# Kernel optimization log

Hardware: AMD Instinct MI355X
Metric: run time of the kernel (lower is better)

Reference implementation:

```python
import jax, jax.numpy as jnp
import numpy as np

EMBED = 768
DIM = 800          # embed + 32 gender features
IN_C = 1024
GRID = 32          # img_size // patch_size(=1)
LN_EPS = 1e-5      # torch nn.LayerNorm default


def setup_inputs() -> dict:
    key = jax.random.key(0)
    ks = jax.random.split(key, 8)
    B = 32
    x = jax.random.normal(ks[0], (B, IN_C, GRID, GRID), dtype=jnp.float32)
    gender_encode = jax.random.normal(ks[1], (B, 32), dtype=jnp.float32)
    # PatchEmbed 1x1 conv (acts as per-pixel linear) + LayerNorm params
    conv_w = jax.random.normal(ks[2], (EMBED, IN_C), dtype=jnp.float32) * (IN_C ** -0.5)
    conv_b = jnp.zeros((EMBED,), dtype=jnp.float32)
    ln_g = jnp.ones((EMBED,), dtype=jnp.float32)
    ln_b = jnp.zeros((EMBED,), dtype=jnp.float32)
    cls_token = jax.random.normal(ks[3], (1, 1, EMBED), dtype=jnp.float32) * 0.02
    # Attention qkv linear (bias=True); proj is never used in the forward path
    qkv_w = jax.random.normal(ks[4], (3 * DIM, DIM), dtype=jnp.float32) * (DIM ** -0.5)
    qkv_b = jnp.zeros((3 * DIM,), dtype=jnp.float32)
    return {
        "x": x, "gender_encode": gender_encode,
        "conv_w": conv_w, "conv_b": conv_b,
        "ln_g": ln_g, "ln_b": ln_b,
        "cls_token": cls_token,
        "qkv_w": qkv_w, "qkv_b": qkv_b,
    }


def _forward(x, gender_encode, conv_w, conv_b, ln_g, ln_b, cls_token, qkv_w, qkv_b):
    B = x.shape[0]
    # PatchEmbed: 1x1 conv stride 1 == per-pixel linear; flatten(2).transpose(1,2)
    p = jnp.einsum('bchw,oc->bhwo', x, conv_w) + conv_b        # [B,32,32,768]
    p = p.reshape(B, GRID * GRID, EMBED)                        # [B,1024,768]
    mu = jnp.mean(p, axis=-1, keepdims=True)
    var = jnp.mean((p - mu) ** 2, axis=-1, keepdims=True)
    p = (p - mu) * jax.lax.rsqrt(var + LN_EPS) * ln_g + ln_b
    # prepend cls token, concat broadcast gender features
    cls = jnp.broadcast_to(cls_token, (B, 1, EMBED))
    t = jnp.concatenate([cls, p], axis=1)                       # [B,1025,768]
    g = jnp.broadcast_to(gender_encode[:, None, :], (B, t.shape[1], 32))
    t = jnp.concatenate([t, g], axis=2)                         # [B,1025,800]
    # Attention (note: self.norm / proj / v are unused in the original forward)
    qkv = t @ qkv_w.T + qkv_b                                   # [B,1025,2400]
    q = qkv[..., 0:DIM]
    k = qkv[..., DIM:2 * DIM]
    scale = DIM ** -0.5
    # only the cls-query row is ever used -> compute just that row
    scores = jnp.einsum('bc,bnc->bn', q[:, 0], k) * scale       # [B,1025]
    attn_cls = jax.nn.softmax(scores[:, 1:], axis=-1)           # [B,1024]
    return attn_cls.reshape(B, 1, GRID, GRID)


def reference(x, gender_encode, conv_w, conv_b, ln_g, ln_b, cls_token, qkv_w, qkv_b):
    return _forward(x, gender_encode, conv_w, conv_b, ln_g, ln_b, cls_token, qkv_w, qkv_b)
```

## Files before the change

kernel.cpp:

```cpp
#include <hip/hip_runtime.h>
#include <hip/hip_bf16.h>

#define EMBED 768
#define DIMQ  800
#define INC   1024
#define NPIX  1024

typedef __bf16 bf16_t;
typedef __bf16 bf16x8 __attribute__((ext_vector_type(8)));
typedef __bf16 bf16x2 __attribute__((ext_vector_type(2)));
typedef float  f32x4  __attribute__((ext_vector_type(4)));

#define GLD_LDS(gp, lp) __builtin_amdgcn_global_load_lds( \
    (const __attribute__((address_space(1))) void*)(gp),  \
    (__attribute__((address_space(3))) void*)(lp), 16, 0, 0)

__global__ __launch_bounds__(256)
void k_prep(const float* __restrict__ x, bf16_t* __restrict__ xT,
            const float* __restrict__ w, bf16_t* __restrict__ cw,
            const float* __restrict__ qkv_w, const float* __restrict__ qkv_b,
            const float* __restrict__ cls, const float* __restrict__ gender,
            float* __restrict__ q0b) {
    __shared__ __align__(16) unsigned int tile[64 * 36];
    const int bi = blockIdx.x;
    const int t  = threadIdx.x;
    if (bi < 8192) {
        const int b  = bi >> 8;
        const int k0 = ((bi >> 4) & 15) * 64;
        const int m0 = (bi & 15) * 64;
        const int m_l = t & 63;
        const int wv  = t >> 6;
        const float* src = x + ((size_t)(b * 1024 + k0 + wv * 16) * 1024) + m0 + m_l;
        bf16x2* trow = (bf16x2*)tile;
#pragma unroll
        for (int i = 0; i < 8; ++i) {
            float a0 = src[(size_t)(2 * i) * 1024];
            float a1 = src[(size_t)(2 * i + 1) * 1024];
            bf16x2 p; p[0] = (bf16_t)a0; p[1] = (bf16_t)a1;
            trow[m_l * 36 + wv * 8 + i] = p;
        }
        __syncthreads();
        const int m_r = t >> 2;
        bf16_t* drow = xT + ((size_t)(b * 1024 + m0 + m_r) * 1024) + k0;
#pragma unroll
        for (int rep = 0; rep < 2; ++rep) {
            int j = (t & 3) + rep * 4;
            bf16x8 v = *(const bf16x8*)&tile[m_r * 36 + j * 4];
            int slot = j ^ (m_r & 7);
            *(bf16x8*)(drow + slot * 8) = v;
        }
    } else if (bi < 8392) {
        const int wv = t >> 6, tl = t & 63;
        const int i = (bi - 8192) * 4 + wv;
        const float* row = qkv_w + (size_t)i * DIMQ;
        float ps = 0.f;
        for (int j = tl; j < EMBED; j += 64) ps += row[j] * cls[j];
#pragma unroll
        for (int off = 1; off < 64; off <<= 1) ps += __shfl_xor(ps, off, 64);
        if (tl < 32) {
            float g = 0.f;
#pragma unroll
            for (int j = 0; j < 32; ++j) g += row[EMBED + j] * gender[tl * 32 + j];
            q0b[tl * DIMQ + i] = ps + g + qkv_b[i];
        }
    } else {
        const int i = (bi - 8392) * 256 + t;
        const int n = i >> 10, k = i & 1023;
        const int s = (k >> 3) & 7;
        const int src_k = (k & ~63) | (((s ^ (n & 7)) & 7) << 3) | (k & 7);
        cw[i] = (bf16_t)w[(size_t)n * 1024 + src_k];
    }
}

__global__ __launch_bounds__(256)
void k_u(const float* __restrict__ qkv_w, const float* __restrict__ q0b,
         const float* __restrict__ ln_g, float* __restrict__ u) {
    __shared__ float q0s[DIMQ];
    __shared__ float sh[8][33];
    int t = threadIdx.x;
    int b  = blockIdx.x / 24;
    int j0 = (blockIdx.x % 24) * 32;
    for (int i = t; i < DIMQ; i += 256) q0s[i] = q0b[b * DIMQ + i];
    __syncthreads();
    int j_l = t & 31, os = t >> 5;
    const float* wk = qkv_w + (size_t)DIMQ * DIMQ;
    const float* wp = wk + (size_t)(os * 100) * DIMQ + j0 + j_l;
    float acc = 0.f;
#pragma unroll 4
    for (int i = 0; i < 100; ++i) acc += wp[(size_t)i * DIMQ] * q0s[os * 100 + i];
    sh[os][j_l] = acc;
    __syncthreads();
    if (t < 32) {
        float s = 0.f;
#pragma unroll
        for (int o = 0; o < 8; ++o) s += sh[o][t];
        u[b * EMBED + j0 + t] = s * ln_g[j0 + t];
    }
}

__global__ __launch_bounds__(256, 3)
void k_main(const bf16_t* __restrict__ xT, const bf16_t* __restrict__ cw,
            const float* __restrict__ conv_b, const float* __restrict__ u,
            float* __restrict__ partial) {
    __shared__ __align__(1024) unsigned char smem[32768 + 3072];

    const int tid = threadIdx.x;
    const int bi = blockIdx.x;
    const int x8 = bi & 7;
    const int s  = bi >> 3;
    const int nt = s % 6;
    const int mt = (s / 6) * 8 + x8;
    const int b  = mt >> 3;
    const int gm = mt * 128;
    const int gn = nt * 128;

    const int wv = tid >> 6;
    const int l  = tid & 63;
    const int lr = l >> 3;
    const int lc = l & 7;

    const int lane = l;
    const int col  = lane & 15;
    const int quad = lane >> 4;
    const int wm   = (wv >> 1) * 64;
    const int wn   = (wv & 1) * 64;

    bf16_t* A = (bf16_t*)smem;
    bf16_t* B = (bf16_t*)(smem + 16384);

    f32x4 C[4][4] = {};

    for (int kt = 0; kt < 16; ++kt) {
        const int ko = kt * 64;
#pragma unroll
        for (int p = 0; p < 4; ++p) {
            const int r = p * 32 + wv * 8 + lr;
            GLD_LDS(xT + (size_t)(gm + r) * 1024 + ko + lc * 8, A + (p * 32 + wv * 8) * 64);
            GLD_LDS(cw + (size_t)(gn + r) * 1024 + ko + lc * 8, B + (p * 32 + wv * 8) * 64);
        }
        __syncthreads();
#pragma unroll
        for (int ks = 0; ks < 2; ++ks) {
            bf16x8 af[4], bg[4];
#pragma unroll
            for (int mi = 0; mi < 4; ++mi) {
                const int r  = wm + mi * 16 + col;
                const int ph = (ks * 4 + quad) ^ (r & 7);
                af[mi] = *(const bf16x8*)(A + r * 64 + ph * 8);
            }
#pragma unroll
            for (int ni = 0; ni < 4; ++ni) {
                const int r  = wn + ni * 16 + col;
                const int ph = (ks * 4 + quad) ^ (r & 7);
                bg[ni] = *(const bf16x8*)(B + r * 64 + ph * 8);
            }
#pragma unroll
            for (int mi = 0; mi < 4; ++mi)
#pragma unroll
                for (int ni = 0; ni < 4; ++ni)
                    C[mi][ni] = __builtin_amdgcn_mfma_f32_16x16x32_bf16(af[mi], bg[ni], C[mi][ni], 0, 0, 0);
        }
        __syncthreads();
    }

    float cb[4], uv[4];
#pragma unroll
    for (int ni = 0; ni < 4; ++ni) {
        const int og = gn + wn + ni * 16 + col;
        cb[ni] = conv_b[og];
        uv[ni] = u[b * EMBED + og];
    }
    float* part = (float*)(smem + 32768);
#pragma unroll
    for (int mi = 0; mi < 4; ++mi)
#pragma unroll
        for (int r = 0; r < 4; ++r) {
            float a = 0.f, sq = 0.f, d = 0.f;
#pragma unroll
            for (int ni = 0; ni < 4; ++ni) {
                float v = C[mi][ni][r] + cb[ni];
                a += v; sq += v * v; d += v * uv[ni];
            }
#pragma unroll
            for (int off = 1; off < 16; off <<= 1) {
                a  += __shfl_xor(a, off, 64);
                sq += __shfl_xor(sq, off, 64);
                d  += __shfl_xor(d, off, 64);
            }
            if (col == 0) {
                const int row = wm + mi * 16 + quad * 4 + r;
                float* pp = part + ((wv & 1) * 128 + row) * 3;
                pp[0] = a; pp[1] = sq; pp[2] = d;
            }
        }
    __syncthreads();
    if (tid < 128) {
        const float* p0 = part + tid * 3;
        const float* p1 = part + (128 + tid) * 3;
        const size_t pix = (size_t)gm + tid;
        partial[(size_t)(0 * 6 + nt) * 32768 + pix] = p0[0] + p1[0];
        partial[(size_t)(1 * 6 + nt) * 32768 + pix] = p0[1] + p1[1];
        partial[(size_t)(2 * 6 + nt) * 32768 + pix] = p0[2] + p1[2];
    }
}

__global__ __launch_bounds__(1024)
void k_final(const float* __restrict__ partial, const float* __restrict__ u,
             float* __restrict__ out) {
    __shared__ float red[16];
    __shared__ float bc[3];
    const int b = blockIdx.x, t = threadIdx.x;
    const int lane = t & 63, wid = t >> 6;

    float pu = (t < EMBED) ? u[b * EMBED + t] : 0.f;
#pragma unroll
    for (int off = 1; off < 64; off <<= 1) pu += __shfl_xor(pu, off, 64);
    if (lane == 0) red[wid] = pu;
    __syncthreads();
    if (t == 0) { float s = 0.f; for (int i = 0; i < 16; ++i) s += red[i]; bc[0] = s; }
    __syncthreads();
    const float Su = bc[0];

    const size_t m = (size_t)b * 1024 + t;
    float S1 = 0.f, S2 = 0.f, S3 = 0.f;
#pragma unroll
    for (int nt = 0; nt < 6; ++nt) {
        S1 += partial[(size_t)(0 * 6 + nt) * 32768 + m];
        S2 += partial[(size_t)(1 * 6 + nt) * 32768 + m];
        S3 += partial[(size_t)(2 * 6 + nt) * 32768 + m];
    }
    const float mu  = S1 * (1.f / 768.f);
    const float var = S2 * (1.f / 768.f) - mu * mu;
    const float sc  = 0.035355339059327376f * (S3 - mu * Su) * rsqrtf(var + 1e-5f);

    float mx = sc;
#pragma unroll
    for (int off = 1; off < 64; off <<= 1) mx = fmaxf(mx, __shfl_xor(mx, off, 64));
    if (lane == 0) red[wid] = mx;
    __syncthreads();
    if (t == 0) { float mm = -1e30f; for (int i = 0; i < 16; ++i) mm = fmaxf(mm, red[i]); bc[1] = mm; }
    __syncthreads();
    const float e = __expf(sc - bc[1]);
    float ss = e;
#pragma unroll
    for (int off = 1; off < 64; off <<= 1) ss += __shfl_xor(ss, off, 64);
    __syncthreads();
    if (lane == 0) red[wid] = ss;
    __syncthreads();
    if (t == 0) { float s = 0.f; for (int i = 0; i < 16; ++i) s += red[i]; bc[2] = s; }
    __syncthreads();
    out[m] = e / bc[2];
}

extern "C" void kernel_launch(void* const* d_in, const int* in_sizes, int n_in,
                              void* d_out, int out_size, void* d_ws, size_t ws_size,
                              hipStream_t stream) {
    const float* x      = (const float*)d_in[0];
    const float* gender = (const float*)d_in[1];
    const float* conv_w = (const float*)d_in[2];
    const float* conv_b = (const float*)d_in[3];
    const float* ln_g   = (const float*)d_in[4];
    const float* cls    = (const float*)d_in[6];
    const float* qkv_w  = (const float*)d_in[7];
    const float* qkv_b  = (const float*)d_in[8];
    float* out = (float*)d_out;

    char* ws = (char*)d_ws;
    bf16_t* cw      = (bf16_t*)ws;
    float*  q0b     = (float*)(ws + 1572864);
    float*  u       = (float*)(ws + 1675264);
    float*  partial = (float*)(ws + 1773568);
    bf16_t* xT      = (bf16_t*)(ws + 4132864);

    hipLaunchKernelGGL(k_prep,  dim3(11464), dim3(256),  0, stream,
                       x, xT, conv_w, cw, qkv_w, qkv_b, cls, gender, q0b);
    hipLaunchKernelGGL(k_u,     dim3(768),   dim3(256),  0, stream, qkv_w, q0b, ln_g, u);
    hipLaunchKernelGGL(k_main,  dim3(1536),  dim3(256),  0, stream, xT, cw, conv_b, u, partial);
    hipLaunchKernelGGL(k_final, dim3(32),    dim3(1024), 0, stream, partial, u, out);
}
```

Before: 303.9 us.

## Vectorize x transpose loads in prep and batch k_u across all batches

The transpose path of k_prep now loads x with 16-byte float4 reads into a swizzled fp32 LDS tile and converts to bf16 when reading the tile back. Before, each thread did scalar strided loads and converted early. k_u is restructured so each of 24 blocks handles 32 output columns for all 32 batches, staging the qkv K-weight and q0 chunks in shared memory. This reads the 800x768 weight once instead of once per batch. The cost is only 24 blocks of 1024 threads, which leaves most of the GPU idle for that kernel.

```diff
diff --git a/kernel.cpp b/kernel.cpp
--- a/kernel.cpp
+++ b/kernel.cpp
@@ -8,7 +8,6 @@
 
 typedef __bf16 bf16_t;
 typedef __bf16 bf16x8 __attribute__((ext_vector_type(8)));
-typedef __bf16 bf16x2 __attribute__((ext_vector_type(2)));
 typedef float  f32x4  __attribute__((ext_vector_type(4)));
 
 #define GLD_LDS(gp, lp) __builtin_amdgcn_global_load_lds( \
@@ -21,33 +20,41 @@
             const float* __restrict__ qkv_w, const float* __restrict__ qkv_b,
             const float* __restrict__ cls, const float* __restrict__ gender,
             float* __restrict__ q0b) {
-    __shared__ __align__(16) unsigned int tile[64 * 36];
+    __shared__ __align__(16) float tile[64 * 64];
     const int bi = blockIdx.x;
     const int t  = threadIdx.x;
     if (bi < 8192) {
         const int b  = bi >> 8;
         const int k0 = ((bi >> 4) & 15) * 64;
         const int m0 = (bi & 15) * 64;
-        const int m_l = t & 63;
-        const int wv  = t >> 6;
-        const float* src = x + ((size_t)(b * 1024 + k0 + wv * 16) * 1024) + m0 + m_l;
-        bf16x2* trow = (bf16x2*)tile;
-#pragma unroll
-        for (int i = 0; i < 8; ++i) {
-            float a0 = src[(size_t)(2 * i) * 1024];
-            float a1 = src[(size_t)(2 * i + 1) * 1024];
-            bf16x2 p; p[0] = (bf16_t)a0; p[1] = (bf16_t)a1;
-            trow[m_l * 36 + wv * 8 + i] = p;
-        }
-        __syncthreads();
-        const int m_r = t >> 2;
-        bf16_t* drow = xT + ((size_t)(b * 1024 + m0 + m_r) * 1024) + k0;
-#pragma unroll
-        for (int rep = 0; rep < 2; ++rep) {
-            int j = (t & 3) + rep * 4;
-            bf16x8 v = *(const bf16x8*)&tile[m_r * 36 + j * 4];
-            int slot = j ^ (m_r & 7);
-            *(bf16x8*)(drow + slot * 8) = v;
+        {
+            const int kl = t >> 4;
+            const int mq = t & 15;
+#pragma unroll
+            for (int r = 0; r < 4; ++r) {
+                const int k = r * 16 + kl;
+                f32x4 v = *(const f32x4*)(x + ((size_t)(b * 1024 + k0 + k) * 1024) + m0 + mq * 4);
+                const int f = ((k >> 3) + (k & 7)) & 15;
+                *(f32x4*)&tile[k * 64 + ((mq ^ f) & 15) * 4] = v;
+            }
+        }
+        __syncthreads();
+        {
+            const int j    = t & 7;
+            const int mrow = t >> 3;
+#pragma unroll
+            for (int rep = 0; rep < 2; ++rep) {
+                const int m = mrow + rep * 32;
+                bf16x8 pk;
+#pragma unroll
+                for (int i = 0; i < 8; ++i) {
+                    const int k = j * 8 + i;
+                    const int f = ((k >> 3) + (k & 7)) & 15;
+                    pk[i] = (bf16_t)tile[k * 64 + (((m >> 2) ^ f) & 15) * 4 + (m & 3)];
+                }
+                const int slot = j ^ (m & 7);
+                *(bf16x8*)(xT + ((size_t)(b * 1024 + m0 + m) * 1024) + k0 + slot * 8) = pk;
+            }
         }
     } else if (bi < 8392) {
         const int wv = t >> 6, tl = t & 63;
@@ -72,30 +79,35 @@
     }
 }
 
-__global__ __launch_bounds__(256)
+__global__ __launch_bounds__(1024)
 void k_u(const float* __restrict__ qkv_w, const float* __restrict__ q0b,
          const float* __restrict__ ln_g, float* __restrict__ u) {
-    __shared__ float q0s[DIMQ];
-    __shared__ float sh[8][33];
-    int t = threadIdx.x;
-    int b  = blockIdx.x / 24;
-    int j0 = (blockIdx.x % 24) * 32;
-    for (int i = t; i < DIMQ; i += 256) q0s[i] = q0b[b * DIMQ + i];
-    __syncthreads();
-    int j_l = t & 31, os = t >> 5;
+    __shared__ float wk_s[160 * 32];
+    __shared__ float q0_s[160 * 33];
+    const int t  = threadIdx.x;
+    const int j0 = blockIdx.x * 32;
+    const int jj = t >> 5, b = t & 31;
     const float* wk = qkv_w + (size_t)DIMQ * DIMQ;
-    const float* wp = wk + (size_t)(os * 100) * DIMQ + j0 + j_l;
-    float acc = 0.f;
-#pragma unroll 4
-    for (int i = 0; i < 100; ++i) acc += wp[(size_t)i * DIMQ] * q0s[os * 100 + i];
-    sh[os][j_l] = acc;
-    __syncthreads();
-    if (t < 32) {
-        float s = 0.f;
-#pragma unroll
-        for (int o = 0; o < 8; ++o) s += sh[o][t];
-        u[b * EMBED + j0 + t] = s * ln_g[j0 + t];
-    }
+    float acc0 = 0.f, acc1 = 0.f;
+    for (int c = 0; c < 5; ++c) {
+        const int o0 = c * 160;
+        __syncthreads();
+#pragma unroll
+        for (int i = 0; i < 5; ++i) {
+            const int idx = i * 1024 + t;
+            const int o  = idx >> 5, jl = idx & 31;
+            wk_s[o * 32 + jl] = wk[(size_t)(o0 + o) * DIMQ + j0 + jl];
+            const int b2 = idx / 160, o2 = idx % 160;
+            q0_s[o2 * 33 + b2] = q0b[b2 * DIMQ + o0 + o2];
+        }
+        __syncthreads();
+#pragma unroll 8
+        for (int o = 0; o < 160; o += 2) {
+            acc0 += wk_s[o * 32 + jj]       * q0_s[o * 33 + b];
+            acc1 += wk_s[(o + 1) * 32 + jj] * q0_s[(o + 1) * 33 + b];
+        }
+    }
+    u[b * EMBED + j0 + jj] = (acc0 + acc1) * ln_g[j0 + jj];
 }
 
 __global__ __launch_bounds__(256, 3)
@@ -274,7 +286,7 @@
 
     hipLaunchKernelGGL(k_prep,  dim3(11464), dim3(256),  0, stream,
                        x, xT, conv_w, cw, qkv_w, qkv_b, cls, gender, q0b);
-    hipLaunchKernelGGL(k_u,     dim3(768),   dim3(256),  0, stream, qkv_w, q0b, ln_g, u);
+    hipLaunchKernelGGL(k_u,     dim3(24),    dim3(1024), 0, stream, qkv_w, q0b, ln_g, u);
     hipLaunchKernelGGL(k_main,  dim3(1536),  dim3(256),  0, stream, xT, cw, conv_b, u, partial);
     hipLaunchKernelGGL(k_final, dim3(32),    dim3(1024), 0, stream, partial, u, out);
 }
```

Result: slower. 315.0 us (+3.6%).
